# Optimization experiments

Measured on AMD Instinct MI355X. Metric: run time of the kernel, lower is better.

Reference implementation:

```python
import jax, jax.numpy as jnp
import numpy as np

# Hyperparameters matching init_kwargs / repo defaults
MARGIN = 0.2
ALPHA = 0.1          # opt.alpha
OT_ITER = 20         # opt.OT_iteration
BETA = 0.5           # IPOT temperature (hardcoded in repo's OT module)
SIM_TYPE = "MISA"    # opt.sim_type_dot
MAX_VIOLATION = True
EPS = 1e-12

N_IMAGE = 128
N_REG = 36
D = 1024
MAX_WORD = 60


def _matchmap_sim(M):
    # M: (n_image, n_regions, n_word)
    if SIM_TYPE == "SISA":
        return M.mean(axis=2).mean(axis=1)
    elif SIM_TYPE == "MISA":
        return M.max(axis=1).mean(axis=1)
    elif SIM_TYPE == "SIMA":
        return M.max(axis=2).mean(axis=1)
    raise ValueError


def _ipot_distance(C, n, m):
    # C: (bs, n, m) cosine-distance cost; IPOT with uniform marginals.
    bs = C.shape[0]
    # Torch code detaches T, so no gradient flows through the iteration.
    A = jnp.exp(-jax.lax.stop_gradient(C) / BETA)

    def body(_, carry):
        T, sigma = carry
        Q = A * T                                            # (bs, n, m)
        delta = 1.0 / (n * jnp.matmul(Q, sigma))             # (bs, n, 1)
        sigma = 1.0 / (m * jnp.matmul(Q.transpose(0, 2, 1), delta))  # (bs, m, 1)
        T = delta * Q * sigma.transpose(0, 2, 1)
        return (T, sigma)

    T0 = jnp.ones((bs, n, m), C.dtype)
    s0 = jnp.ones((bs, m, 1), C.dtype) / m
    T, _ = jax.lax.fori_loop(0, OT_ITER, body, (T0, s0))
    T = jax.lax.stop_gradient(T)
    # batch_trace(C^T T) == sum(C * T) per batch element
    return -jnp.sum(C * T, axis=(1, 2))                      # (bs,)


def _scores(im, s, cap_lens):
    n_reg = im.shape[1]
    imn = im / (jnp.linalg.norm(im, axis=2, keepdims=True) + EPS)
    lens = np.asarray(cap_lens)
    sims, sims_ot = [], []
    for i in range(s.shape[0]):  # ragged per-caption loop (as in original)
        n_word = int(lens[i])
        cap = s[i, :n_word, :]                               # (w, d)
        # matchmap: bmm(images, cap^T) -> (n_image, n_regions, n_word)
        M = jnp.einsum('brd,wd->brw', im, cap)
        sims.append(_matchmap_sim(M))
        capn = cap / (jnp.linalg.norm(cap, axis=1, keepdims=True) + EPS)
        # cost_matrix_batch_torch(cap^T, img^T).transpose -> (n_image, n_reg, n_word)
        C = 1.0 - jnp.einsum('brd,wd->brw', imn, capn)
        sims_ot.append(_ipot_distance(C, n_reg, n_word))
    return jnp.stack(sims, axis=1), jnp.stack(sims_ot, axis=1)  # (n_img, n_cap)


def _loss(im, s, cap_lens):
    scores, scores_ot = _scores(im, s, cap_lens)
    n = scores.shape[0]
    eye = jnp.eye(n, dtype=bool)

    def costs(sc):
        d = jnp.diag(sc)[:, None]                            # (n, 1)
        cs = jnp.clip(MARGIN + sc - d, 0.0)                  # caption-side
        ci = jnp.clip(MARGIN + sc - d.T, 0.0)                # image-side
        cs = jnp.where(eye, 0.0, cs)
        ci = jnp.where(eye, 0.0, ci)
        return cs, ci

    cost_s, cost_im = costs(scores)
    cost_s_ot, cost_im_ot = costs(scores_ot)
    cost_s = cost_s + ALPHA * cost_s_ot
    cost_im = cost_im + ALPHA * cost_im_ot
    if MAX_VIOLATION:
        cost_s = cost_s.max(axis=1)
        cost_im = cost_im.max(axis=0)
        cost_s_ot = cost_s_ot.max(axis=1)
        cost_im_ot = cost_im_ot.max(axis=0)
    return (cost_s.sum() + cost_im.sum(), cost_s_ot.sum() + cost_im_ot.sum())


def setup_inputs() -> dict:
    key = jax.random.key(0)
    k1, k2, k3 = jax.random.split(key, 3)
    im = jax.random.normal(k1, (N_IMAGE, N_REG, D), dtype=jnp.float32)
    s = jax.random.normal(k2, (N_IMAGE, MAX_WORD, D), dtype=jnp.float32)
    rng = np.random.default_rng(0)
    s_l = np.asarray(rng.integers(10, MAX_WORD + 1, size=N_IMAGE), dtype=np.int64)
    x = jax.random.normal(k3, (1,), dtype=jnp.float32)  # unused by forward math
    return {"im": im, "s": s, "s_l": s_l, "x": x}


def reference(im, s, s_l, x):
    return _loss(im, s, s_l)
```

## Files before the change

kernel.cpp:

```cpp
#include <hip/hip_runtime.h>
#include <hip/hip_bf16.h>
#include <math.h>

#define N_IMAGE 128
#define N_REG   36
#define DIM     1024
#define MAX_WORD 60
#define OT_ITERS 20
#define MARGIN_F 0.2f
#define ALPHA_F  0.1f
#define EPS_F    1e-12f

typedef short bf16x8 __attribute__((ext_vector_type(8)));
typedef float f32x4  __attribute__((ext_vector_type(4)));
typedef float f32x2  __attribute__((ext_vector_type(2)));


__device__ __forceinline__ unsigned int pkbf2(float a, float b) {
    union { __hip_bfloat162 h2; unsigned int u; } cv;
    cv.h2 = __float22bfloat162_rn(make_float2(a, b));
    return cv.u;
}
__device__ __forceinline__ float lo16(unsigned int u) { return __int_as_float((int)(u << 16)); }
__device__ __forceinline__ float hi16(unsigned int u) { return __int_as_float((int)(u & 0xFFFF0000u)); }

#define SWZ(x, pat) __int_as_float(__builtin_amdgcn_ds_swizzle(__float_as_int(x), (pat)))
#define BPERM(a, x) __int_as_float(__builtin_amdgcn_ds_bpermute((a), __float_as_int(x)))
#define DPPADD(x, ctrl) \
    ((x) + __int_as_float(__builtin_amdgcn_update_dpp(0, __float_as_int(x), (ctrl), 0xf, 0xf, true)))

__device__ __forceinline__ float bfly16_sum(float x) {
    x = DPPADD(x, 0xB1);
    x = DPPADD(x, 0x4E);
    x = DPPADD(x, 0x124);
    x = DPPADD(x, 0x128);
    return x;
}
__device__ __forceinline__ float bfly64_sum(float x, int xaddr) {
    x = bfly16_sum(x);
    x += SWZ(x, 0x401F);
    x += BPERM(xaddr, x);
    return x;
}


__global__ void norms_kernel(const float* __restrict__ im, const float* __restrict__ s,
                             float* __restrict__ inv_im, float* __restrict__ inv_cap,
                             float* __restrict__ out, int conv,
                             unsigned short* __restrict__ im16,
                             unsigned short* __restrict__ s16) {
    if (blockIdx.x == 0 && threadIdx.x == 0) { out[0] = 0.0f; out[1] = 0.0f; }
    const int NIM = N_IMAGE * N_REG;
    const int NS  = N_IMAGE * MAX_WORD;
    int row  = blockIdx.x * 4 + (threadIdx.x >> 6);
    int lane = threadIdx.x & 63;
    if (row >= NIM + NS) return;
    const bool isim = (row < NIM);
    const float* base = isim ? (im + (size_t)row * DIM)
                             : (s  + (size_t)(row - NIM) * DIM);
    unsigned short* dst = isim ? (im16 + (size_t)row * DIM)
                               : (s16  + (size_t)(row - NIM) * DIM);
    const float4* b4 = (const float4*)base;
    float acc = 0.0f;
    for (int k = lane; k < DIM / 4; k += 64) {
        float4 v = b4[k];
        acc += v.x * v.x + v.y * v.y + v.z * v.z + v.w * v.w;
        if (conv) {
            uint2 w2; w2.x = pkbf2(v.x, v.y); w2.y = pkbf2(v.z, v.w);
            *(uint2*)(dst + k * 4) = w2;
        }
    }
    for (int off = 32; off; off >>= 1) acc += __shfl_down(acc, off, 64);
    if (lane == 0) {
        float inv = 1.0f / (sqrtf(acc) + EPS_F);
        if (isim) inv_im[row] = inv;
        else      inv_cap[row - NIM] = inv;
    }
}


template <bool BF16IN, int CT>
__device__ __forceinline__ void pair_body(
    const float* __restrict__ im, const float* __restrict__ s,
    const unsigned short* __restrict__ im16, const unsigned short* __restrict__ s16,
    char* smem, const float* invImS, const float* invCapS,
    int cap, int b0, int m,
    float* __restrict__ S, float* __restrict__ SOT) {

    const int tid  = threadIdx.x;
    const int lane = tid & 63;
    const int wv   = tid >> 6;
    const int q    = lane >> 4;
    const int l15  = lane & 15;
    const int q4   = tid & 15;
    const int row0 = tid >> 4;
    const int xaddr = ((lane ^ 32) << 2);

    const float mf    = (float)m;
    const float inv_m = 1.0f / mf;

    const char* sA = smem;
    const char* sB = smem + 27648;

    f32x4 acc[3 * CT];
    #pragma unroll
    for (int t = 0; t < 3 * CT; ++t) acc[t] = (f32x4){0.f, 0.f, 0.f, 0.f};

    for (int c = 0; c < 16; ++c) {
        const int col = c * 64 + q4 * 4;
        #pragma unroll
        for (int img = 0; img < 4; ++img) {
            #pragma unroll
            for (int j = 0; j < 3; ++j) {
                const int r = row0 + 16 * j;
                if (j < 2 || row0 < 4) {
                    const size_t ro = (size_t)(b0 * 36 + img * 36 + r) * 1024 + col;
                    uint2 w2;
                    if (BF16IN) {
                        w2 = *(const uint2*)(im16 + ro);
                    } else {
                        float4 v = *(const float4*)(im + ro);
                        w2.x = pkbf2(v.x, v.y); w2.y = pkbf2(v.z, v.w);
                    }
                    *(uint2*)(smem + (img * 48 + r) * 144 + q4 * 8) = w2;
                }
            }
        }
        #pragma unroll
        for (int j = 0; j < CT; ++j) {
            const int r = row0 + 16 * j;
            if (CT < 4 || j < 3 || row0 < 12) {
                const size_t ro = (size_t)(cap * 60 + r) * 1024 + col;
                uint2 w2;
                if (BF16IN) {
                    w2 = *(const uint2*)(s16 + ro);
                } else {
                    float4 v = *(const float4*)(s + ro);
                    w2.x = pkbf2(v.x, v.y); w2.y = pkbf2(v.z, v.w);
                }
                *(uint2*)(smem + (192 + r) * 144 + q4 * 8) = w2;
            }
        }
        __syncthreads();
        #pragma unroll
        for (int h = 0; h < 2; ++h) {
            bf16x8 bfr[CT];
            #pragma unroll
            for (int ct = 0; ct < CT; ++ct)
                bfr[ct] = *(const bf16x8*)(sB + (ct * 16 + l15) * 144 + h * 64 + q * 16);
            #pragma unroll
            for (int rt = 0; rt < 3; ++rt) {
                bf16x8 afr = *(const bf16x8*)(sA + (wv * 48 + rt * 16 + l15) * 144 + h * 64 + q * 16);
                #pragma unroll
                for (int ct = 0; ct < CT; ++ct)
                    acc[rt * CT + ct] = __builtin_amdgcn_mfma_f32_16x16x32_bf16(
                        afr, bfr[ct], acc[rt * CT + ct], 0, 0, 0);
            }
        }
        __syncthreads();
    }

    constexpr int PK = (CT + 1) / 2;
    float icap[CT]; bool vw[CT];
    #pragma unroll
    for (int ct = 0; ct < CT; ++ct) {
        const int w = ct * 16 + l15;
        vw[ct]   = (w < m);
        icap[ct] = (w < 60) ? invCapS[w] : 0.0f;
    }

    unsigned int apk[12][PK];
    float mxv[CT];
    #pragma unroll
    for (int ct = 0; ct < CT; ++ct) mxv[ct] = -3e38f;

    #pragma unroll
    for (int j = 0; j < 12; ++j) {
        const int rt = j >> 2, p = j & 3;
        const int r  = rt * 16 + q * 4 + p;
        const bool rowok = (rt < 2) || (q == 0);
        const float iir = rowok ? invImS[wv * 36 + (r < 36 ? r : 0)] : 0.0f;
        float av[CT];
        #pragma unroll
        for (int ct = 0; ct < CT; ++ct) {
            const float Mv = acc[rt * CT + ct][p];
            mxv[ct] = fmaxf(mxv[ct], rowok ? Mv : -3e38f);
            const float cv = 1.0f - Mv * iir * icap[ct];
            const bool ok  = rowok && vw[ct];
            av[ct] = ok ? __expf(-2.0f * cv) : 0.0f;
        }
        #pragma unroll
        for (int pk = 0; pk < PK; ++pk)
            apk[j][pk] = pkbf2(av[2 * pk], (2 * pk + 1 < CT) ? av[2 * pk + 1] : 0.0f);
    }

    {
        const int baddr = l15 << 2;
        #pragma unroll
        for (int pk = 0; pk < PK; ++pk) {
            const int r0 = __builtin_amdgcn_ds_bpermute(baddr, (int)apk[8][pk]);
            const int r1 = __builtin_amdgcn_ds_bpermute(baddr, (int)apk[9][pk]);
            const int r2 = __builtin_amdgcn_ds_bpermute(baddr, (int)apk[10][pk]);
            const int r3 = __builtin_amdgcn_ds_bpermute(baddr, (int)apk[11][pk]);
            const int lo = (q & 1) ? r1 : r0;
            const int hi = (q & 1) ? r3 : r2;
            apk[8][pk] = (unsigned int)((q & 2) ? hi : lo);
        }
    }

    const int b = b0 + wv;
    {
        float sp = 0.0f;
        #pragma unroll
        for (int ct = 0; ct < CT; ++ct) {
            float v = mxv[ct];
            v = fmaxf(v, SWZ(v, 0x401F));
            v = fmaxf(v, BPERM(xaddr, v));
            sp += vw[ct] ? v : 0.0f;
        }
        sp = bfly64_sum(sp, xaddr);
        if (lane == 0) S[(size_t)b * N_IMAGE + cap] = sp * inv_m * 0.25f;
    }

    f32x2 t2[9][PK];
    f32x2 sig2[PK];
    #pragma unroll
    for (int pk = 0; pk < PK; ++pk) {
        const bool v0 = vw[2 * pk];
        const bool v1 = (2 * pk + 1 < CT) && vw[2 * pk + 1];
        sig2[pk].x = v0 ? inv_m : 0.0f;
        sig2[pk].y = v1 ? inv_m : 0.0f;
        #pragma unroll
        for (int j = 0; j < 9; ++j) {
            t2[j][pk].x = v0 ? mf : 0.0f;
            t2[j][pk].y = v1 ? mf : 0.0f;
        }
    }

    for (int it = 0; it < OT_ITERS; ++it) {
        f32x2 s2[PK], csum[PK];
        #pragma unroll
        for (int pk = 0; pk < PK; ++pk) {
            s2[pk]   = sig2[pk] * sig2[pk];
            csum[pk] = (f32x2){0.0f, 0.0f};
        }
        #pragma unroll
        for (int j = 0; j < 9; ++j) {
            f32x2 at[PK];
            #pragma unroll
            for (int pk = 0; pk < PK; ++pk) {
                f32x2 a2;
                a2.x = lo16(apk[j][pk]);
                a2.y = hi16(apk[j][pk]);
                at[pk] = a2 * t2[j][pk];
            }
            f32x2 u2 = at[0] * s2[0];
            #pragma unroll
            for (int pk = 1; pk < PK; ++pk) u2 += at[pk] * s2[pk];
            const float R  = bfly16_sum(u2.x + u2.y);
            const float dl = __builtin_amdgcn_rcpf(36.0f * R);
            f32x2 dl2; dl2.x = dl; dl2.y = dl;
            #pragma unroll
            for (int pk = 0; pk < PK; ++pk) {
                const f32x2 tn = at[pk] * (dl2 * sig2[pk]);
                t2[j][pk] = tn;
                csum[pk] += tn;
            }
        }
        #pragma unroll
        for (int pk = 0; pk < PK; ++pk) {
            float cx = csum[pk].x;
            cx += SWZ(cx, 0x401F);
            cx += BPERM(xaddr, cx);
            float cy = csum[pk].y;
            cy += SWZ(cy, 0x401F);
            cy += BPERM(xaddr, cy);
            const bool v0 = vw[2 * pk];
            const bool v1 = (2 * pk + 1 < CT) && vw[2 * pk + 1];
            sig2[pk].x = v0 ? __builtin_amdgcn_rcpf(mf * cx) : 0.0f;
            sig2[pk].y = v1 ? __builtin_amdgcn_rcpf(mf * cy) : 0.0f;
        }
    }

    {
        float pp = 0.0f;
        #pragma unroll
        for (int j = 0; j < 9; ++j) {
            #pragma unroll
            for (int pk = 0; pk < PK; ++pk) {
                const float ax = lo16(apk[j][pk]);
                const float cvx = -0.5f * __logf(fmaxf(ax, 1e-30f));
                pp = fmaf(cvx, t2[j][pk].x * sig2[pk].x, pp);
                if (2 * pk + 1 < CT) {
                    const float ay = hi16(apk[j][pk]);
                    const float cvy = -0.5f * __logf(fmaxf(ay, 1e-30f));
                    pp = fmaf(cvy, t2[j][pk].y * sig2[pk].y, pp);
                }
            }
        }
        pp = bfly64_sum(pp, xaddr);
        if (lane == 0) SOT[(size_t)b * N_IMAGE + cap] = -pp;
    }
}

template <bool BF16IN>
__global__ __launch_bounds__(256, 4)
void pair_kernel(const float* __restrict__ im, const float* __restrict__ s,
                 const unsigned short* __restrict__ im16,
                 const unsigned short* __restrict__ s16,
                 const int* __restrict__ s_l,
                 const float* __restrict__ inv_im, const float* __restrict__ inv_cap,
                 float* __restrict__ S, float* __restrict__ SOT) {
    const int cap = blockIdx.x;
    const int b0  = blockIdx.y * 4;
    const int tid = threadIdx.x;

    __shared__ __align__(16) char smem[36864];
    __shared__ float invImS[144];
    __shared__ float invCapS[60];

    if (tid < 144) invImS[tid] = inv_im[b0 * 36 + tid];
    else if (tid < 204) invCapS[tid - 144] = inv_cap[cap * 60 + (tid - 144)];

    const int m = s_l[cap];

    {
        float4 z = make_float4(0.f, 0.f, 0.f, 0.f);
        #pragma unroll
        for (int j = 0; j < 9; ++j)
            *(float4*)(smem + (tid + j * 256) * 16) = z;
    }
    __syncthreads();

    const int CT = __builtin_amdgcn_readfirstlane((m + 15) >> 4);
    switch (CT) {
    case 1: pair_body<BF16IN, 1>(im, s, im16, s16, smem, invImS, invCapS, cap, b0, m, S, SOT); break;
    case 2: pair_body<BF16IN, 2>(im, s, im16, s16, smem, invImS, invCapS, cap, b0, m, S, SOT); break;
    case 3: pair_body<BF16IN, 3>(im, s, im16, s16, smem, invImS, invCapS, cap, b0, m, S, SOT); break;
    default: pair_body<BF16IN, 4>(im, s, im16, s16, smem, invImS, invCapS, cap, b0, m, S, SOT); break;
    }
}


__global__ void loss_kernel(const float* __restrict__ S, const float* __restrict__ SOT,
                            float* __restrict__ out) {
    const int j = blockIdx.x;
    const int t = threadIdx.x;
    __shared__ float sh[4][2];
    const float db  = S[j * 129];
    const float dob = SOT[j * 129];
    float rv = 0.f, rov = 0.f, cv = 0.f, cov = 0.f;
    if (t != j) {
        float cs  = fmaxf(0.0f, MARGIN_F + S[j * 128 + t] - db);
        float cso = fmaxf(0.0f, MARGIN_F + SOT[j * 128 + t] - dob);
        rv = cs + ALPHA_F * cso;  rov = cso;
        float ci  = fmaxf(0.0f, MARGIN_F + S[t * 128 + j] - db);
        float cio = fmaxf(0.0f, MARGIN_F + SOT[t * 128 + j] - dob);
        cv = ci + ALPHA_F * cio;  cov = cio;
    }
    for (int off = 32; off; off >>= 1) {
        rv  = fmaxf(rv,  __shfl_down(rv,  off, 64));
        rov = fmaxf(rov, __shfl_down(rov, off, 64));
        cv  = fmaxf(cv,  __shfl_down(cv,  off, 64));
        cov = fmaxf(cov, __shfl_down(cov, off, 64));
    }
    if ((t & 63) == 0) {
        sh[0][t >> 6] = rv; sh[1][t >> 6] = rov;
        sh[2][t >> 6] = cv; sh[3][t >> 6] = cov;
    }
    __syncthreads();
    if (t == 0) {
        float a0 = fmaxf(sh[0][0], sh[0][1]) + fmaxf(sh[2][0], sh[2][1]);
        float a1 = fmaxf(sh[1][0], sh[1][1]) + fmaxf(sh[3][0], sh[3][1]);
        atomicAdd(&out[0], a0);
        atomicAdd(&out[1], a1);
    }
}

extern "C" void kernel_launch(void* const* d_in, const int* in_sizes, int n_in,
                              void* d_out, int out_size, void* d_ws, size_t ws_size,
                              hipStream_t stream) {
    const float* im  = (const float*)d_in[0];
    const float* s   = (const float*)d_in[1];
    const int*   s_l = (const int*)d_in[2];
    float* out = (float*)d_out;
    float* ws  = (float*)d_ws;

    float* inv_im  = ws;
    float* inv_cap = ws + 4608;
    float* S       = ws + 12288;
    float* SOT     = ws + 12288 + 16384;
    unsigned short* im16 = (unsigned short*)((char*)d_ws + 180224);
    unsigned short* s16  = im16 + (size_t)N_IMAGE * N_REG * DIM;
    const size_t need = 180224 +
        ((size_t)N_IMAGE * N_REG * DIM + (size_t)N_IMAGE * MAX_WORD * DIM) * 2;
    const int fast = (ws_size >= need) ? 1 : 0;

    norms_kernel<<<dim3((4608 + 7680) / 4), dim3(256), 0, stream>>>(
        im, s, inv_im, inv_cap, out, fast, im16, s16);
    if (fast)
        pair_kernel<true><<<dim3(N_IMAGE, N_IMAGE / 4), dim3(256), 0, stream>>>(
            im, s, im16, s16, s_l, inv_im, inv_cap, S, SOT);
    else
        pair_kernel<false><<<dim3(N_IMAGE, N_IMAGE / 4), dim3(256), 0, stream>>>(
            im, s, im16, s16, s_l, inv_im, inv_cap, S, SOT);
    loss_kernel<<<dim3(N_IMAGE), dim3(128), 0, stream>>>(S, SOT, out);
}
```

Baseline: 312.2 us.

## Pre-pack bf16 operands into MFMA fragment layout and load directly to registers

Adds a pack kernel that converts images and captions to bf16 in a layout already matching the 16x16x32 MFMA fragment order, with zero-padded rows, and computes the row norms in the same pass. The fast pair kernel then loads fragments straight from global memory into registers with double buffering across k-chunks. This drops the shared-memory staging and the two barriers per chunk. It costs more workspace for the padded layout and relies on L2 to serve the repeated caption and image reads across blocks.

```diff
diff --git a/kernel.cpp b/kernel.cpp
--- a/kernel.cpp
+++ b/kernel.cpp
@@ -11,6 +11,10 @@
 #define ALPHA_F  0.1f
 #define EPS_F    1e-12f
 
+#define APAN  16384
+#define AIMG  (3 * APAN)
+#define BCAP  (4 * APAN)
+
 typedef short bf16x8 __attribute__((ext_vector_type(8)));
 typedef float f32x4  __attribute__((ext_vector_type(4)));
 typedef float f32x2  __attribute__((ext_vector_type(2)));
@@ -44,11 +48,77 @@
 }
 
 
+__global__ __launch_bounds__(256) void pack_kernel(
+    const float* __restrict__ im, const float* __restrict__ s,
+    float* __restrict__ inv_im, float* __restrict__ inv_cap,
+    float* __restrict__ out,
+    unsigned short* __restrict__ imp, unsigned short* __restrict__ sp) {
+
+    const int pid = blockIdx.x;
+    const int tid = threadIdx.x;
+    if (pid == 0 && tid == 0) { out[0] = 0.0f; out[1] = 0.0f; }
+
+    const int w = tid >> 6, lane = tid & 63, q = lane >> 4, l15 = lane & 15;
+    const bool isim = (pid < 384);
+    int obj, p, nvalid;
+    const float* src;
+    unsigned short* dst;
+    if (isim) {
+        obj = pid / 3; p = pid % 3;
+        src = im + (size_t)obj * 36 * DIM;
+        dst = imp + (size_t)obj * AIMG + (size_t)p * APAN;
+        nvalid = 36;
+    } else {
+        const int k = pid - 384;
+        obj = k >> 2; p = k & 3;
+        src = s + (size_t)obj * 60 * DIM;
+        dst = sp + (size_t)obj * BCAP + (size_t)p * APAN;
+        nvalid = 60;
+    }
+    const int row = p * 16 + l15;
+    const bool valid = (row < nvalid);
+
+    float ss = 0.0f;
+    #pragma unroll
+    for (int i = 0; i < 4; ++i) {
+        const int c = w * 4 + i;
+        #pragma unroll
+        for (int h = 0; h < 2; ++h) {
+            float4 v0 = make_float4(0.f, 0.f, 0.f, 0.f), v1 = v0;
+            if (valid) {
+                const float* rp = src + (size_t)row * DIM + c * 64 + h * 32 + q * 8;
+                v0 = *(const float4*)rp;
+                v1 = *(const float4*)(rp + 4);
+            }
+            ss += v0.x * v0.x + v0.y * v0.y + v0.z * v0.z + v0.w * v0.w
+                + v1.x * v1.x + v1.y * v1.y + v1.z * v1.z + v1.w * v1.w;
+            uint4 o;
+            o.x = pkbf2(v0.x, v0.y); o.y = pkbf2(v0.z, v0.w);
+            o.z = pkbf2(v1.x, v1.y); o.w = pkbf2(v1.z, v1.w);
+            *(uint4*)(dst + (size_t)c * 1024 + h * 512 + q * 128 + l15 * 8) = o;
+        }
+    }
+    const int xaddr = ((lane ^ 32) << 2);
+    ss += SWZ(ss, 0x401F);
+    ss += BPERM(xaddr, ss);
+    __shared__ float sh[4][16];
+    if (lane < 16) sh[w][lane] = ss;
+    __syncthreads();
+    if (tid < 16) {
+        const float t = sh[0][tid] + sh[1][tid] + sh[2][tid] + sh[3][tid];
+        const int r = p * 16 + tid;
+        if (r < nvalid) {
+            const float inv = 1.0f / (sqrtf(t) + EPS_F);
+            if (isim) inv_im[obj * 36 + r] = inv;
+            else      inv_cap[obj * 60 + r] = inv;
+        }
+    }
+}
+
+
 __global__ void norms_kernel(const float* __restrict__ im, const float* __restrict__ s,
                              float* __restrict__ inv_im, float* __restrict__ inv_cap,
-                             float* __restrict__ out, int conv,
-                             unsigned short* __restrict__ im16,
-                             unsigned short* __restrict__ s16) {
+                             float* __restrict__ out) {
     if (blockIdx.x == 0 && threadIdx.x == 0) { out[0] = 0.0f; out[1] = 0.0f; }
     const int NIM = N_IMAGE * N_REG;
     const int NS  = N_IMAGE * MAX_WORD;
@@ -58,17 +128,11 @@
     const bool isim = (row < NIM);
     const float* base = isim ? (im + (size_t)row * DIM)
                              : (s  + (size_t)(row - NIM) * DIM);
-    unsigned short* dst = isim ? (im16 + (size_t)row * DIM)
-                               : (s16  + (size_t)(row - NIM) * DIM);
     const float4* b4 = (const float4*)base;
     float acc = 0.0f;
     for (int k = lane; k < DIM / 4; k += 64) {
         float4 v = b4[k];
         acc += v.x * v.x + v.y * v.y + v.z * v.z + v.w * v.w;
-        if (conv) {
-            uint2 w2; w2.x = pkbf2(v.x, v.y); w2.y = pkbf2(v.z, v.w);
-            *(uint2*)(dst + k * 4) = w2;
-        }
     }
     for (int off = 32; off; off >>= 1) acc += __shfl_down(acc, off, 64);
     if (lane == 0) {
@@ -79,86 +143,19 @@
 }
 
 
-template <bool BF16IN, int CT>
-__device__ __forceinline__ void pair_body(
-    const float* __restrict__ im, const float* __restrict__ s,
-    const unsigned short* __restrict__ im16, const unsigned short* __restrict__ s16,
-    char* smem, const float* invImS, const float* invCapS,
-    int cap, int b0, int m,
-    float* __restrict__ S, float* __restrict__ SOT) {
+template <int CT>
+__device__ __forceinline__ void ot_epilogue(
+    f32x4 (&acc)[3 * CT], const float* invImS, const float* invCapS,
+    int cap, int b0, int m, float* __restrict__ S, float* __restrict__ SOT) {
 
     const int tid  = threadIdx.x;
     const int lane = tid & 63;
     const int wv   = tid >> 6;
     const int q    = lane >> 4;
     const int l15  = lane & 15;
-    const int q4   = tid & 15;
-    const int row0 = tid >> 4;
     const int xaddr = ((lane ^ 32) << 2);
-
     const float mf    = (float)m;
     const float inv_m = 1.0f / mf;
-
-    const char* sA = smem;
-    const char* sB = smem + 27648;
-
-    f32x4 acc[3 * CT];
-    #pragma unroll
-    for (int t = 0; t < 3 * CT; ++t) acc[t] = (f32x4){0.f, 0.f, 0.f, 0.f};
-
-    for (int c = 0; c < 16; ++c) {
-        const int col = c * 64 + q4 * 4;
-        #pragma unroll
-        for (int img = 0; img < 4; ++img) {
-            #pragma unroll
-            for (int j = 0; j < 3; ++j) {
-                const int r = row0 + 16 * j;
-                if (j < 2 || row0 < 4) {
-                    const size_t ro = (size_t)(b0 * 36 + img * 36 + r) * 1024 + col;
-                    uint2 w2;
-                    if (BF16IN) {
-                        w2 = *(const uint2*)(im16 + ro);
-                    } else {
-                        float4 v = *(const float4*)(im + ro);
-                        w2.x = pkbf2(v.x, v.y); w2.y = pkbf2(v.z, v.w);
-                    }
-                    *(uint2*)(smem + (img * 48 + r) * 144 + q4 * 8) = w2;
-                }
-            }
-        }
-        #pragma unroll
-        for (int j = 0; j < CT; ++j) {
-            const int r = row0 + 16 * j;
-            if (CT < 4 || j < 3 || row0 < 12) {
-                const size_t ro = (size_t)(cap * 60 + r) * 1024 + col;
-                uint2 w2;
-                if (BF16IN) {
-                    w2 = *(const uint2*)(s16 + ro);
-                } else {
-                    float4 v = *(const float4*)(s + ro);
-                    w2.x = pkbf2(v.x, v.y); w2.y = pkbf2(v.z, v.w);
-                }
-                *(uint2*)(smem + (192 + r) * 144 + q4 * 8) = w2;
-            }
-        }
-        __syncthreads();
-        #pragma unroll
-        for (int h = 0; h < 2; ++h) {
-            bf16x8 bfr[CT];
-            #pragma unroll
-            for (int ct = 0; ct < CT; ++ct)
-                bfr[ct] = *(const bf16x8*)(sB + (ct * 16 + l15) * 144 + h * 64 + q * 16);
-            #pragma unroll
-            for (int rt = 0; rt < 3; ++rt) {
-                bf16x8 afr = *(const bf16x8*)(sA + (wv * 48 + rt * 16 + l15) * 144 + h * 64 + q * 16);
-                #pragma unroll
-                for (int ct = 0; ct < CT; ++ct)
-                    acc[rt * CT + ct] = __builtin_amdgcn_mfma_f32_16x16x32_bf16(
-                        afr, bfr[ct], acc[rt * CT + ct], 0, 0, 0);
-            }
-        }
-        __syncthreads();
-    }
 
     constexpr int PK = (CT + 1) / 2;
     float icap[CT]; bool vw[CT];
@@ -303,18 +300,169 @@
     }
 }
 
-template <bool BF16IN>
+
+template <int CT>
+__device__ __forceinline__ void pair_body_fast(
+    const unsigned short* __restrict__ imp, const unsigned short* __restrict__ sp,
+    const float* invImS, const float* invCapS,
+    int cap, int b0, int m,
+    float* __restrict__ S, float* __restrict__ SOT) {
+
+    const int tid  = threadIdx.x;
+    const int lane = tid & 63;
+    const int wv   = tid >> 6;
+    const int q    = lane >> 4;
+    const int l15  = lane & 15;
+
+    const unsigned short* Ab = imp + (size_t)(b0 + wv) * AIMG + (q * 128 + l15 * 8);
+    const unsigned short* Bb = sp  + (size_t)cap * BCAP        + (q * 128 + l15 * 8);
+
+    f32x4 acc[3 * CT];
+    #pragma unroll
+    for (int t = 0; t < 3 * CT; ++t) acc[t] = (f32x4){0.f, 0.f, 0.f, 0.f};
+
+    bf16x8 a0[3], bf0[CT], a1[3], bf1[CT];
+    #pragma unroll
+    for (int rt = 0; rt < 3; ++rt) a0[rt] = *(const bf16x8*)(Ab + rt * APAN);
+    #pragma unroll
+    for (int ct = 0; ct < CT; ++ct) bf0[ct] = *(const bf16x8*)(Bb + ct * APAN);
+
+    #pragma unroll 1
+    for (int c = 0; c < 16; ++c) {
+        const unsigned short* Ac = Ab + c * 1024;
+        const unsigned short* Bc = Bb + c * 1024;
+        #pragma unroll
+        for (int rt = 0; rt < 3; ++rt) a1[rt] = *(const bf16x8*)(Ac + rt * APAN + 512);
+        #pragma unroll
+        for (int ct = 0; ct < CT; ++ct) bf1[ct] = *(const bf16x8*)(Bc + ct * APAN + 512);
+        #pragma unroll
+        for (int rt = 0; rt < 3; ++rt)
+            #pragma unroll
+            for (int ct = 0; ct < CT; ++ct)
+                acc[rt * CT + ct] = __builtin_amdgcn_mfma_f32_16x16x32_bf16(
+                    a0[rt], bf0[ct], acc[rt * CT + ct], 0, 0, 0);
+        const int cn = (c < 15) ? c + 1 : 15;
+        const unsigned short* An = Ab + cn * 1024;
+        const unsigned short* Bn = Bb + cn * 1024;
+        #pragma unroll
+        for (int rt = 0; rt < 3; ++rt) a0[rt] = *(const bf16x8*)(An + rt * APAN);
+        #pragma unroll
+        for (int ct = 0; ct < CT; ++ct) bf0[ct] = *(const bf16x8*)(Bn + ct * APAN);
+        #pragma unroll
+        for (int rt = 0; rt < 3; ++rt)
+            #pragma unroll
+            for (int ct = 0; ct < CT; ++ct)
+                acc[rt * CT + ct] = __builtin_amdgcn_mfma_f32_16x16x32_bf16(
+                    a1[rt], bf1[ct], acc[rt * CT + ct], 0, 0, 0);
+    }
+
+    __syncthreads();
+    ot_epilogue<CT>(acc, invImS, invCapS, cap, b0, m, S, SOT);
+}
+
 __global__ __launch_bounds__(256, 4)
-void pair_kernel(const float* __restrict__ im, const float* __restrict__ s,
-                 const unsigned short* __restrict__ im16,
-                 const unsigned short* __restrict__ s16,
-                 const int* __restrict__ s_l,
-                 const float* __restrict__ inv_im, const float* __restrict__ inv_cap,
-                 float* __restrict__ S, float* __restrict__ SOT) {
+void pair_fast(const unsigned short* __restrict__ imp,
+               const unsigned short* __restrict__ sp,
+               const int* __restrict__ s_l,
+               const float* __restrict__ inv_im, const float* __restrict__ inv_cap,
+               float* __restrict__ S, float* __restrict__ SOT) {
     const int cap = blockIdx.x;
     const int b0  = blockIdx.y * 4;
     const int tid = threadIdx.x;
 
+    __shared__ float invImS[144];
+    __shared__ float invCapS[60];
+    if (tid < 144) invImS[tid] = inv_im[b0 * 36 + tid];
+    else if (tid < 204) invCapS[tid - 144] = inv_cap[cap * 60 + (tid - 144)];
+
+    const int m  = s_l[cap];
+    const int CT = __builtin_amdgcn_readfirstlane((m + 15) >> 4);
+    switch (CT) {
+    case 1: pair_body_fast<1>(imp, sp, invImS, invCapS, cap, b0, m, S, SOT); break;
+    case 2: pair_body_fast<2>(imp, sp, invImS, invCapS, cap, b0, m, S, SOT); break;
+    case 3: pair_body_fast<3>(imp, sp, invImS, invCapS, cap, b0, m, S, SOT); break;
+    default: pair_body_fast<4>(imp, sp, invImS, invCapS, cap, b0, m, S, SOT); break;
+    }
+}
+
+
+template <int CT>
+__device__ __forceinline__ void pair_body_slow(
+    const float* __restrict__ im, const float* __restrict__ s,
+    char* smem, const float* invImS, const float* invCapS,
+    int cap, int b0, int m,
+    float* __restrict__ S, float* __restrict__ SOT) {
+
+    const int tid  = threadIdx.x;
+    const int lane = tid & 63;
+    const int wv   = tid >> 6;
+    const int q    = lane >> 4;
+    const int l15  = lane & 15;
+    const int q4   = tid & 15;
+    const int row0 = tid >> 4;
+
+    const char* sA = smem;
+    const char* sB = smem + 27648;
+
+    f32x4 acc[3 * CT];
+    #pragma unroll
+    for (int t = 0; t < 3 * CT; ++t) acc[t] = (f32x4){0.f, 0.f, 0.f, 0.f};
+
+    for (int c = 0; c < 16; ++c) {
+        const int col = c * 64 + q4 * 4;
+        #pragma unroll
+        for (int img = 0; img < 4; ++img) {
+            #pragma unroll
+            for (int j = 0; j < 3; ++j) {
+                const int r = row0 + 16 * j;
+                if (j < 2 || row0 < 4) {
+                    const size_t ro = (size_t)(b0 * 36 + img * 36 + r) * 1024 + col;
+                    float4 v = *(const float4*)(im + ro);
+                    uint2 w2; w2.x = pkbf2(v.x, v.y); w2.y = pkbf2(v.z, v.w);
+                    *(uint2*)(smem + (img * 48 + r) * 144 + q4 * 8) = w2;
+                }
+            }
+        }
+        #pragma unroll
+        for (int j = 0; j < CT; ++j) {
+            const int r = row0 + 16 * j;
+            if (CT < 4 || j < 3 || row0 < 12) {
+                const size_t ro = (size_t)(cap * 60 + r) * 1024 + col;
+                float4 v = *(const float4*)(s + ro);
+                uint2 w2; w2.x = pkbf2(v.x, v.y); w2.y = pkbf2(v.z, v.w);
+                *(uint2*)(smem + (192 + r) * 144 + q4 * 8) = w2;
+            }
+        }
+        __syncthreads();
+        #pragma unroll
+        for (int h = 0; h < 2; ++h) {
+            bf16x8 bfr[CT];
+            #pragma unroll
+            for (int ct = 0; ct < CT; ++ct)
+                bfr[ct] = *(const bf16x8*)(sB + (ct * 16 + l15) * 144 + h * 64 + q * 16);
+            #pragma unroll
+            for (int rt = 0; rt < 3; ++rt) {
+                bf16x8 afr = *(const bf16x8*)(sA + (wv * 48 + rt * 16 + l15) * 144 + h * 64 + q * 16);
+                #pragma unroll
+                for (int ct = 0; ct < CT; ++ct)
+                    acc[rt * CT + ct] = __builtin_amdgcn_mfma_f32_16x16x32_bf16(
+                        afr, bfr[ct], acc[rt * CT + ct], 0, 0, 0);
+            }
+        }
+        __syncthreads();
+    }
+    ot_epilogue<CT>(acc, invImS, invCapS, cap, b0, m, S, SOT);
+}
+
+__global__ __launch_bounds__(256, 4)
+void pair_slow(const float* __restrict__ im, const float* __restrict__ s,
+               const int* __restrict__ s_l,
+               const float* __restrict__ inv_im, const float* __restrict__ inv_cap,
+               float* __restrict__ S, float* __restrict__ SOT) {
+    const int cap = blockIdx.x;
+    const int b0  = blockIdx.y * 4;
+    const int tid = threadIdx.x;
+
     __shared__ __align__(16) char smem[36864];
     __shared__ float invImS[144];
     __shared__ float invCapS[60];
@@ -323,7 +471,6 @@
     else if (tid < 204) invCapS[tid - 144] = inv_cap[cap * 60 + (tid - 144)];
 
     const int m = s_l[cap];
-
     {
         float4 z = make_float4(0.f, 0.f, 0.f, 0.f);
         #pragma unroll
@@ -334,10 +481,10 @@
 
     const int CT = __builtin_amdgcn_readfirstlane((m + 15) >> 4);
     switch (CT) {
-    case 1: pair_body<BF16IN, 1>(im, s, im16, s16, smem, invImS, invCapS, cap, b0, m, S, SOT); break;
-    case 2: pair_body<BF16IN, 2>(im, s, im16, s16, smem, invImS, invCapS, cap, b0, m, S, SOT); break;
-    case 3: pair_body<BF16IN, 3>(im, s, im16, s16, smem, invImS, invCapS, cap, b0, m, S, SOT); break;
-    default: pair_body<BF16IN, 4>(im, s, im16, s16, smem, invImS, invCapS, cap, b0, m, S, SOT); break;
+    case 1: pair_body_slow<1>(im, s, smem, invImS, invCapS, cap, b0, m, S, SOT); break;
+    case 2: pair_body_slow<2>(im, s, smem, invImS, invCapS, cap, b0, m, S, SOT); break;
+    case 3: pair_body_slow<3>(im, s, smem, invImS, invCapS, cap, b0, m, S, SOT); break;
+    default: pair_body_slow<4>(im, s, smem, invImS, invCapS, cap, b0, m, S, SOT); break;
     }
 }
 
@@ -390,19 +537,22 @@
     float* inv_cap = ws + 4608;
     float* S       = ws + 12288;
     float* SOT     = ws + 12288 + 16384;
-    unsigned short* im16 = (unsigned short*)((char*)d_ws + 180224);
-    unsigned short* s16  = im16 + (size_t)N_IMAGE * N_REG * DIM;
+    unsigned short* imp = (unsigned short*)((char*)d_ws + 180224);
+    unsigned short* sp  = imp + (size_t)N_IMAGE * AIMG;
     const size_t need = 180224 +
-        ((size_t)N_IMAGE * N_REG * DIM + (size_t)N_IMAGE * MAX_WORD * DIM) * 2;
+        ((size_t)N_IMAGE * AIMG + (size_t)N_IMAGE * BCAP) * 2;
     const int fast = (ws_size >= need) ? 1 : 0;
 
-    norms_kernel<<<dim3((4608 + 7680) / 4), dim3(256), 0, stream>>>(
-        im, s, inv_im, inv_cap, out, fast, im16, s16);
-    if (fast)
-        pair_kernel<true><<<dim3(N_IMAGE, N_IMAGE / 4), dim3(256), 0, stream>>>(
-            im, s, im16, s16, s_l, inv_im, inv_cap, S, SOT);
-    else
-        pair_kernel<false><<<dim3(N_IMAGE, N_IMAGE / 4), dim3(256), 0, stream>>>(
-            im, s, im16, s16, s_l, inv_im, inv_cap, S, SOT);
+    if (fast) {
+        pack_kernel<<<dim3(896), dim3(256), 0, stream>>>(
+            im, s, inv_im, inv_cap, out, imp, sp);
+        pair_fast<<<dim3(N_IMAGE, N_IMAGE / 4), dim3(256), 0, stream>>>(
+            imp, sp, s_l, inv_im, inv_cap, S, SOT);
+    } else {
+        norms_kernel<<<dim3((4608 + 7680) / 4), dim3(256), 0, stream>>>(
+            im, s, inv_im, inv_cap, out);
+        pair_slow<<<dim3(N_IMAGE, N_IMAGE / 4), dim3(256), 0, stream>>>(
+            im, s, s_l, inv_im, inv_cap, S, SOT);
+    }
     loss_kernel<<<dim3(N_IMAGE), dim3(128), 0, stream>>>(S, SOT, out);
 }
```

After: 283.6 us. 1.1x faster.
